# Kernel tuning notes

Measured on AMD Instinct MI355X. Metric: run time of the kernel, lower is better.

Reference implementation:

```python
import jax, jax.numpy as jnp
import numpy as np

B, N, T, FD = 128, 64, 20, 2
E, H, A = 16, 32, 32
DB, DH = 30.0, 30.0
NB, NHD = 12, 12  # 360/30 bearing and heading bins
DOMAIN_INIT = 5.0
EPS = 1e-12


def setup_inputs() -> dict:
    key = jax.random.key(0)
    ks = jax.random.split(key, 20)
    rn = lambda k, s, sc=0.1: (jax.random.normal(k, s) * sc).astype(jnp.float32)
    return {
        'x': jax.random.normal(ks[0], (B, N, T, FD), jnp.float32),
        'dmat': jax.random.uniform(ks[1], (B, N, T, N), jnp.float32) * 10.0,
        'bmat': jax.random.uniform(ks[2], (B, N, T, N), jnp.float32) * 360.0,
        'hmat': jax.random.uniform(ks[3], (B, N, T, N), jnp.float32) * 360.0,
        'mask': jnp.ones((B, N, T), jnp.float32),
        'emb_W': rn(ks[4], (E, FD)), 'emb_b': rn(ks[5], (E,)),
        'W_ih': rn(ks[6], (4 * H, E)), 'W_hh': rn(ks[7], (4 * H, H)),
        'b_ih': rn(ks[8], (4 * H,)), 'b_hh': rn(ks[9], (4 * H,)),
        'domain': jnp.full((NB, NHD), DOMAIN_INIT, jnp.float32),
        'enc2att_W': rn(ks[10], (A, H)), 'enc2att_b': rn(ks[11], (A,)),
        'spa_W': rn(ks[12], (A, 2 * A)), 'spa_b': rn(ks[13], (A,)),
        'att2enc_W': rn(ks[14], (H, A)), 'att2enc_b': rn(ks[15], (H,)),
        'cls_W': rn(ks[16], (1, H)), 'cls_b': rn(ks[17], (1,)),
        'h0': jax.random.normal(ks[18], (B * N, H), jnp.float32),
        'c0': jax.random.normal(ks[19], (B * N, H), jnp.float32),
    }


def _forward(x, dmat, bmat, hmat, mask, emb_W, emb_b, W_ih, W_hh, b_ih, b_hh,
             domain, enc2att_W, enc2att_b, spa_W, spa_b, att2enc_W, att2enc_b,
             cls_W, cls_b, h0, c0):
    # input embedding: [B,N,T,F] -> [T, B*N, E] (time-major for scan)
    xe = jnp.einsum('bntf,ef->bnte', x, emb_W) + emb_b
    xe = jnp.moveaxis(xe.reshape(B * N, T, E), 1, 0)
    dm_t = jnp.moveaxis(dmat, 2, 0)   # [T,B,N,N]
    bm_t = jnp.moveaxis(bmat, 2, 0)
    hm_t = jnp.moveaxis(hmat, 2, 0)
    mk_t = jnp.moveaxis(mask, 2, 0)   # [T,B,N]
    eye = jnp.eye(N, dtype=x.dtype)

    def step(carry, inputs):
        h, c = carry                     # [B*N, H]
        xt, dm, bm, hm, mk = inputs
        # single-step LSTM cell (torch gate order i,f,g,o)
        g = xt @ W_ih.T + b_ih + h @ W_hh.T + b_hh
        i, f, gg, o = jnp.split(g, 4, axis=-1)
        c = jax.nn.sigmoid(f) * c + jax.nn.sigmoid(i) * jnp.tanh(gg)
        h = jax.nn.sigmoid(o) * jnp.tanh(c)
        # project encoder state to attention space: [B,N,A]
        a = h.reshape(B, N, H) @ enc2att_W.T + enc2att_b
        # spatial attention weights from distance/bearing/heading edge feats
        ib = jnp.clip(jnp.floor(bm / DB), 0, NB - 1).astype(jnp.int32)
        ih = jnp.clip(jnp.floor(hm / DH), 0, NHD - 1).astype(jnp.int32)
        w = jax.nn.relu(domain[ib, ih] - dm)               # [B,N,N]
        w = w * mk[:, :, None] * mk[:, None, :] * (1.0 - eye)
        w = w / (jnp.sum(w, axis=-1, keepdims=True) + EPS)
        att = jnp.einsum('bij,bjd->bid', w, a)
        z = jnp.tanh(jnp.concatenate([a, att], axis=-1) @ spa_W.T + spa_b)
        h = (z @ att2enc_W.T + att2enc_b).reshape(B * N, H)
        return (h, c), None

    (h, c), _ = jax.lax.scan(step, (h0, c0), (xe, dm_t, bm_t, hm_t, mk_t))
    scores = jnp.tanh(h.reshape(B, N, H) @ cls_W.T + cls_b)
    return jax.nn.sigmoid(scores)  # [B, N, 1]


def reference(x, dmat, bmat, hmat, mask, emb_W, emb_b, W_ih, W_hh, b_ih, b_hh,
              domain, enc2att_W, enc2att_b, spa_W, spa_b, att2enc_W, att2enc_b,
              cls_W, cls_b, h0, c0):
    return _forward(x, dmat, bmat, hmat, mask, emb_W, emb_b, W_ih, W_hh, b_ih,
                    b_hh, domain, enc2att_W, enc2att_b, spa_W, spa_b,
                    att2enc_W, att2enc_b, cls_W, cls_b, h0, c0)
```

## Files before the change

### kernel.cpp

```cpp
#include <hip/hip_runtime.h>
#include <math.h>

#define T_STEPS 20

typedef _Float16 half8 __attribute__((ext_vector_type(8)));
typedef __fp16 fp16x2 __attribute__((ext_vector_type(2)));
typedef float f32x4 __attribute__((ext_vector_type(4)));

__device__ __forceinline__ float sigm(float v) {
  return __builtin_amdgcn_rcpf(1.0f + __expf(-v));
}
__device__ __forceinline__ float tanh_f(float v) {
  return 1.0f - 2.0f * __builtin_amdgcn_rcpf(1.0f + __expf(2.0f * v));
}

__device__ __forceinline__ void barrier_lgkm() {
  asm volatile("s_waitcnt lgkmcnt(0)" ::: "memory");
  __builtin_amdgcn_s_barrier();
  asm volatile("" ::: "memory");
}

__device__ __forceinline__ int2 pkpair(const f32x4 D) {
  const fp16x2 p0 = __builtin_amdgcn_cvt_pkrtz(D[0], D[1]);
  const fp16x2 p1 = __builtin_amdgcn_cvt_pkrtz(D[2], D[3]);
  int2 r;
  r.x = __builtin_bit_cast(int, p0);
  r.y = __builtin_bit_cast(int, p1);
  return r;
}

__global__ __launch_bounds__(1024)
void traj_disc(const float* __restrict__ x, const float* __restrict__ dmat,
               const float* __restrict__ bmat, const float* __restrict__ hmat,
               const float* __restrict__ maskp,
               const float* __restrict__ embW, const float* __restrict__ embb,
               const float* __restrict__ Wih, const float* __restrict__ Whh,
               const float* __restrict__ bih, const float* __restrict__ bhh,
               const float* __restrict__ dom,
               const float* __restrict__ e2aW, const float* __restrict__ e2ab,
               const float* __restrict__ spaW, const float* __restrict__ spab,
               const float* __restrict__ a2eW, const float* __restrict__ a2eb,
               const float* __restrict__ clsW, const float* __restrict__ clsb,
               const float* __restrict__ h0p, const float* __restrict__ c0p,
               float* __restrict__ out)
{
  __shared__ __align__(16) _Float16 sgw[128*40];
  __shared__ __align__(16) _Float16 sgwc[128*40];
  __shared__ __align__(16) float4   sgmb[128];
  __shared__ __align__(16) _Float16 sESaT[32*40];
  __shared__ __align__(16) _Float16 sEStT[32*40];
  __shared__ float bz[32];
  __shared__ float sdom[144];
  __shared__ float sm[1280];
  __shared__ float sclsc[32];
  __shared__ float sclsb2[1];
  __shared__ __align__(16) _Float16 sH[64*40];
  __shared__ __align__(16) _Float16 swA[64*72];
  __shared__ __align__(16) _Float16 swB[64*72];
  __shared__ __align__(16) _Float16 sz_[64*40];
  __shared__ __align__(16) _Float16 sqb[8*16*72 + 1440];

  const int tid = threadIdx.x;
  const int b = blockIdx.x;
  const int w = tid >> 6;
  const int l = tid & 63;
  const int quad = l >> 4;
  const int n16 = l & 15;
  const int i8 = (tid >= 512) ? ((tid - 512) >> 3) : 0;
  const int s8 = tid & 7;

  for (int idx = tid; idx < 4096; idx += 1024) sgw[(idx >> 5)*40 + (idx & 31)] = (_Float16)Whh[idx];
  {
    const int g = tid >> 3, kb = (tid & 7) << 2;
    float a0 = 0.f, a1 = 0.f, a2 = 0.f, a3 = 0.f;
    #pragma unroll
    for (int h = 0; h < 32; ++h) {
      const float wv = Whh[g*32 + h];
      a0 = fmaf(wv, a2eW[h*32 + kb + 0], a0);
      a1 = fmaf(wv, a2eW[h*32 + kb + 1], a1);
      a2 = fmaf(wv, a2eW[h*32 + kb + 2], a2);
      a3 = fmaf(wv, a2eW[h*32 + kb + 3], a3);
    }
    sgwc[g*40 + kb + 0] = (_Float16)a0; sgwc[g*40 + kb + 1] = (_Float16)a1;
    sgwc[g*40 + kb + 2] = (_Float16)a2; sgwc[g*40 + kb + 3] = (_Float16)a3;
  }
  if (tid < 128) {
    float m0 = 0.f, m1 = 0.f, b0 = bih[tid] + bhh[tid];
    #pragma unroll
    for (int e = 0; e < 16; ++e) {
      float wv_ = Wih[tid*16 + e];
      m0 = fmaf(wv_, embW[2*e],   m0);
      m1 = fmaf(wv_, embW[2*e+1], m1);
      b0 = fmaf(wv_, embb[e],     b0);
    }
    float bn = b0;
    #pragma unroll
    for (int h = 0; h < 32; ++h) bn = fmaf(Whh[tid*32 + h], a2eb[h], bn);
    sgmb[tid] = make_float4(m0, m1, b0, bn);
  }
  {
    const int zk = tid >> 5, hc = tid & 31;
    float sa_ = 0.f, st_ = 0.f;
    #pragma unroll
    for (int a = 0; a < 32; ++a) {
      const float ev = e2aW[a*32 + hc];
      sa_ = fmaf(spaW[zk*64 + a],      ev, sa_);
      st_ = fmaf(spaW[zk*64 + 32 + a], ev, st_);
    }
    sESaT[zk*40 + hc] = (_Float16)sa_;
    sEStT[zk*40 + hc] = (_Float16)st_;
  }
  if (tid < 32) {
    float acc = spab[tid];
    #pragma unroll
    for (int a = 0; a < 32; ++a)
      acc = fmaf(e2ab[a], spaW[tid*64 + a] + spaW[tid*64 + 32 + a], acc);
    bz[tid] = acc;
    float cc = 0.f;
    #pragma unroll
    for (int h = 0; h < 32; ++h) cc = fmaf(clsW[h], a2eW[h*32 + tid], cc);
    sclsc[tid] = cc;
  }
  if (tid == 0) {
    float cb = clsb[0];
    #pragma unroll
    for (int h = 0; h < 32; ++h) cb = fmaf(clsW[h], a2eb[h], cb);
    sclsb2[0] = cb;
  }
  if (tid < 144) sdom[tid] = dom[tid];
  for (int idx = tid; idx < 1280; idx += 1024)
    sm[idx] = maskp[(size_t)b*1280 + (size_t)(idx & 63)*20 + (idx >> 6)];
  for (int idx = tid; idx < 2048; idx += 1024) sz_[(idx >> 5)*40 + (idx & 31)] = (_Float16)h0p[(size_t)b*2048 + idx];

  f32x4 ccell;
  float2 xA, xB, xC, xD;
  f32x4 dmv0, dmv1, bmv0, bmv1, hmv0, hmv1;
  const float* xpre = nullptr;
  size_t ebp = 0;
  const int r = w >> 1, c = w & 1;
  if (w < 8) {
    const int hh = 16*c + n16;
    #pragma unroll
    for (int reg = 0; reg < 4; ++reg)
      ccell[reg] = c0p[(size_t)b*2048 + (size_t)(16*r + 4*quad + reg)*32 + hh];
    xpre = x + (size_t)(b*64 + 16*r + 4*quad) * 40;
    xA = *(const float2*)(xpre +   0);
    xB = *(const float2*)(xpre +  40);
    xC = *(const float2*)(xpre +  80);
    xD = *(const float2*)(xpre + 120);
  } else {
    ebp = ((size_t)(b*64 + i8)*20)*64 + (size_t)(s8*8);
    dmv0 = *(const f32x4*)(dmat + ebp); dmv1 = *(const f32x4*)(dmat + ebp + 4);
    bmv0 = *(const f32x4*)(bmat + ebp); bmv1 = *(const f32x4*)(bmat + ebp + 4);
    hmv0 = *(const f32x4*)(hmat + ebp); hmv1 = *(const f32x4*)(hmat + ebp + 4);
  }
  __syncthreads();

#define WC(dst, k, dmv, bmv, hmv, jof) { \
  int ib_ = (int)floorf(bmv[k] * (1.0f/30.0f)); ib_ = ib_ < 0 ? 0 : (ib_ > 11 ? 11 : ib_); \
  int ih_ = (int)floorf(hmv[k] * (1.0f/30.0f)); ih_ = ih_ < 0 ? 0 : (ih_ > 11 ? 11 : ih_); \
  float w_ = fmaxf(sdom[ib_*12 + ih_] - dmv[k], 0.0f) * (mi_ * sm[tloc*64 + 8*s8 + (jof)]); \
  w_ = (8*s8 + (jof) == i8) ? 0.0f : w_; dst[k] = w_; rs += w_; }

#define DO_3A(tn_, swdst) { \
  const int tloc = (tn_); \
  const float mi_ = sm[tloc*64 + i8]; \
  f32x4 wnA, wnB; float rs = 0.0f; \
  WC(wnA,0,dmv0,bmv0,hmv0,0) WC(wnA,1,dmv0,bmv0,hmv0,1) \
  WC(wnA,2,dmv0,bmv0,hmv0,2) WC(wnA,3,dmv0,bmv0,hmv0,3) \
  WC(wnB,0,dmv1,bmv1,hmv1,4) WC(wnB,1,dmv1,bmv1,hmv1,5) \
  WC(wnB,2,dmv1,bmv1,hmv1,6) WC(wnB,3,dmv1,bmv1,hmv1,7) \
  rs += __shfl_xor(rs, 1); rs += __shfl_xor(rs, 2); rs += __shfl_xor(rs, 4); \
  const float inv_ = __builtin_amdgcn_rcpf(rs + 1e-12f); \
  half8 hw; \
  hw[0] = (_Float16)(wnA[0]*inv_); hw[1] = (_Float16)(wnA[1]*inv_); \
  hw[2] = (_Float16)(wnA[2]*inv_); hw[3] = (_Float16)(wnA[3]*inv_); \
  hw[4] = (_Float16)(wnB[0]*inv_); hw[5] = (_Float16)(wnB[1]*inv_); \
  hw[6] = (_Float16)(wnB[2]*inv_); hw[7] = (_Float16)(wnB[3]*inv_); \
  *(half8*)((swdst) + i8*72 + s8*8) = hw; }

  half8 EStB{}, ESaB{};
  float bzv = 0.f;
  if (w < 8) {
    EStB = *(const half8*)(sEStT + (16*c + n16)*40 + quad*8);
    ESaB = *(const half8*)(sESaT + (16*c + n16)*40 + quad*8);
    bzv = bz[16*c + n16];
  } else {
    DO_3A(0, swA);
    const size_t eb1 = ebp + 64;
    dmv0 = *(const f32x4*)(dmat + eb1); dmv1 = *(const f32x4*)(dmat + eb1 + 4);
    bmv0 = *(const f32x4*)(bmat + eb1); bmv1 = *(const f32x4*)(bmat + eb1 + 4);
    hmv0 = *(const f32x4*)(hmat + eb1); hmv1 = *(const f32x4*)(hmat + eb1 + 4);
  }

  #pragma unroll 1
  for (int t = 0; t < T_STEPS; ++t) {
    if (w < 8) {
      const _Float16* Bbase = (t == 0) ? sgw : sgwc;
      const half8 Af = *(const half8*)(sz_ + (16*r + n16)*40 + quad*8);
      f32x4 G0, G1, G2, G3;
#define OP1Q(Gq, q) { \
      const int c_ = 2*(q) + c; \
      const half8 Bf = *(const half8*)(Bbase + (16*c_ + n16)*40 + quad*8); \
      const float4 mb = sgmb[16*c_ + n16]; \
      const float bb = (t == 0) ? mb.z : mb.w; \
      f32x4 Cv; \
      Cv[0] = fmaf(xA.x, mb.x, fmaf(xA.y, mb.y, bb)); \
      Cv[1] = fmaf(xB.x, mb.x, fmaf(xB.y, mb.y, bb)); \
      Cv[2] = fmaf(xC.x, mb.x, fmaf(xC.y, mb.y, bb)); \
      Cv[3] = fmaf(xD.x, mb.x, fmaf(xD.y, mb.y, bb)); \
      Gq = __builtin_amdgcn_mfma_f32_16x16x32_f16(Af, Bf, Cv, 0, 0, 0); }
      OP1Q(G0, 0) OP1Q(G1, 1) OP1Q(G2, 2) OP1Q(G3, 3)
#undef OP1Q
      const int hh = 16*c + n16;
      #pragma unroll
      for (int reg = 0; reg < 4; ++reg) {
        const float cc = fmaf(sigm(G1[reg]), ccell[reg], sigm(G0[reg]) * tanh_f(G2[reg]));
        ccell[reg] = cc;
        sH[(16*r + 4*quad + reg)*40 + hh] = (_Float16)(sigm(G3[reg]) * tanh_f(cc));
      }
      const int tn2 = ((t < T_STEPS - 1) ? t + 1 : t) << 1;
      xA = *(const float2*)(xpre + tn2);
      xB = *(const float2*)(xpre + tn2 +  40);
      xC = *(const float2*)(xpre + tn2 +  80);
      xD = *(const float2*)(xpre + tn2 + 120);
    } else {
      const int tn = (t < T_STEPS - 1) ? t + 1 : t;
      _Float16* swn = ((t + 1) & 1) ? swB : swA;
      DO_3A(tn, swn);
      const int tp = (t < T_STEPS - 2) ? t + 2 : T_STEPS - 1;
      const size_t eb2 = ebp + (size_t)tp*64;
      dmv0 = *(const f32x4*)(dmat + eb2); dmv1 = *(const f32x4*)(dmat + eb2 + 4);
      bmv0 = *(const f32x4*)(bmat + eb2); bmv1 = *(const f32x4*)(bmat + eb2 + 4);
      hmv0 = *(const f32x4*)(hmat + eb2); hmv1 = *(const f32x4*)(hmat + eb2 + 4);
    }
    barrier_lgkm();

    if (w < 8) {
      const _Float16* swr = (t & 1) ? swB : swA;
      _Float16* qb = sqb + w*(16*72);
      const half8 a0 = *(const half8*)(sH + (     n16)*40 + quad*8);
      const half8 a1 = *(const half8*)(sH + (16 + n16)*40 + quad*8);
      const half8 a2 = *(const half8*)(sH + (32 + n16)*40 + quad*8);
      const half8 a3 = *(const half8*)(sH + (48 + n16)*40 + quad*8);
      const half8 aP = *(const half8*)(sH + (16*r + n16)*40 + quad*8);
      const half8 A0 = *(const half8*)(swr + (16*r + n16)*72 + quad*8);
      const half8 A1 = *(const half8*)(swr + (16*r + n16)*72 + 32 + quad*8);
      f32x4 Pv; Pv[0] = bzv; Pv[1] = bzv; Pv[2] = bzv; Pv[3] = bzv;
      Pv = __builtin_amdgcn_mfma_f32_16x16x32_f16(aP, ESaB, Pv, 0, 0, 0);
      const f32x4 Z4 = {0.f, 0.f, 0.f, 0.f};
      const f32x4 D0 = __builtin_amdgcn_mfma_f32_16x16x32_f16(a0, EStB, Z4, 0, 0, 0);
      const f32x4 D1 = __builtin_amdgcn_mfma_f32_16x16x32_f16(a1, EStB, Z4, 0, 0, 0);
      const f32x4 D2 = __builtin_amdgcn_mfma_f32_16x16x32_f16(a2, EStB, Z4, 0, 0, 0);
      const f32x4 D3 = __builtin_amdgcn_mfma_f32_16x16x32_f16(a3, EStB, Z4, 0, 0, 0);
      *(int2*)(qb + n16*72 +  0 + 4*quad) = pkpair(D0);
      *(int2*)(qb + n16*72 + 16 + 4*quad) = pkpair(D1);
      *(int2*)(qb + n16*72 + 32 + 4*quad) = pkpair(D2);
      *(int2*)(qb + n16*72 + 48 + 4*quad) = pkpair(D3);
      const half8 Bf0 = *(const half8*)(qb + n16*72 + 8*quad);
      const half8 Bf1 = *(const half8*)(qb + n16*72 + 32 + 8*quad);
      Pv = __builtin_amdgcn_mfma_f32_16x16x32_f16(A0, Bf0, Pv, 0, 0, 0);
      Pv = __builtin_amdgcn_mfma_f32_16x16x32_f16(A1, Bf1, Pv, 0, 0, 0);
      const int nd = 16*r + 4*quad;
      sz_[(nd+0)*40 + 16*c + n16] = (_Float16)tanh_f(Pv[0]);
      sz_[(nd+1)*40 + 16*c + n16] = (_Float16)tanh_f(Pv[1]);
      sz_[(nd+2)*40 + 16*c + n16] = (_Float16)tanh_f(Pv[2]);
      sz_[(nd+3)*40 + 16*c + n16] = (_Float16)tanh_f(Pv[3]);
    }
    barrier_lgkm();
  }

#undef DO_3A
#undef WC

  if (tid < 64) {
    float acc = sclsb2[0];
    #pragma unroll
    for (int k = 0; k < 32; ++k) acc = fmaf((float)sz_[tid*40 + k], sclsc[k], acc);
    out[(size_t)b*64 + tid] = sigm(tanh_f(acc));
  }
}

extern "C" void kernel_launch(void* const* d_in, const int* in_sizes, int n_in,
                              void* d_out, int out_size, void* d_ws, size_t ws_size,
                              hipStream_t stream) {
  (void)in_sizes; (void)n_in; (void)d_ws; (void)ws_size; (void)out_size;
  const float* x    = (const float*)d_in[0];
  const float* dmat = (const float*)d_in[1];
  const float* bmat = (const float*)d_in[2];
  const float* hmat = (const float*)d_in[3];
  const float* mask = (const float*)d_in[4];
  const float* embW = (const float*)d_in[5];
  const float* embb = (const float*)d_in[6];
  const float* Wih  = (const float*)d_in[7];
  const float* Whh  = (const float*)d_in[8];
  const float* bih  = (const float*)d_in[9];
  const float* bhh  = (const float*)d_in[10];
  const float* dom  = (const float*)d_in[11];
  const float* e2aW = (const float*)d_in[12];
  const float* e2ab = (const float*)d_in[13];
  const float* spaW = (const float*)d_in[14];
  const float* spab = (const float*)d_in[15];
  const float* a2eW = (const float*)d_in[16];
  const float* a2eb = (const float*)d_in[17];
  const float* clsW = (const float*)d_in[18];
  const float* clsb = (const float*)d_in[19];
  const float* h0   = (const float*)d_in[20];
  const float* c0   = (const float*)d_in[21];
  float* out = (float*)d_out;

  traj_disc<<<dim3(128), dim3(1024), 0, stream>>>(
      x, dmat, bmat, hmat, mask, embW, embb, Wih, Whh, bih, bhh, dom,
      e2aW, e2ab, spaW, spab, a2eW, a2eb, clsW, clsb, h0, c0, out);
}
```

Before: 209.1 us.

## Pack two batches per block and fold exp scaling into gate weights

Each 1024-thread block now processes two batch elements with 512 threads each, and every wave performs both the edge-weight construction and the LSTM/attention MFMA work instead of specializing waves. Gate weights and biases are prescaled by -log2e (or 2·log2e for the tanh gate) so the activations use a raw v_exp_f32. Bearing and heading bin indices are now truncated without floor or clamp. This removes the wave specialization and some transcendental overhead, but halves the grid and lengthens each wave's per-step serial work, and it relies on angles staying in [0,360).

```diff
diff --git a/kernel.cpp b/kernel.cpp
--- a/kernel.cpp
+++ b/kernel.cpp
@@ -2,11 +2,15 @@
 #include <math.h>
 
 #define T_STEPS 20
+#define LOG2E 1.44269504088896f
 
 typedef _Float16 half8 __attribute__((ext_vector_type(8)));
 typedef __fp16 fp16x2 __attribute__((ext_vector_type(2)));
 typedef float f32x4 __attribute__((ext_vector_type(4)));
 
+__device__ __forceinline__ float exp2_f(float v) {
+  float r; asm("v_exp_f32 %0, %1" : "=v"(r) : "v"(v)); return r;
+}
 __device__ __forceinline__ float sigm(float v) {
   return __builtin_amdgcn_rcpf(1.0f + __expf(-v));
 }
@@ -51,27 +55,34 @@
   __shared__ __align__(16) _Float16 sEStT[32*40];
   __shared__ float bz[32];
   __shared__ float sdom[144];
-  __shared__ float sm[1280];
   __shared__ float sclsc[32];
   __shared__ float sclsb2[1];
-  __shared__ __align__(16) _Float16 sH[64*40];
-  __shared__ __align__(16) _Float16 swA[64*72];
-  __shared__ __align__(16) _Float16 swB[64*72];
-  __shared__ __align__(16) _Float16 sz_[64*40];
-  __shared__ __align__(16) _Float16 sqb[8*16*72 + 1440];
+  __shared__ float sm[2][1280];
+  __shared__ __align__(16) _Float16 sH[2][64*40];
+  __shared__ __align__(16) _Float16 swA[2][64*72];
+  __shared__ __align__(16) _Float16 swB[2][64*72];
+  __shared__ __align__(16) _Float16 sz_[2][64*40];
+  __shared__ __align__(16) _Float16 sqb[2][8*16*72];
 
   const int tid = threadIdx.x;
-  const int b = blockIdx.x;
-  const int w = tid >> 6;
+  const int g2 = tid >> 9;
+  const int btid = tid & 511;
+  const int bb = (blockIdx.x << 1) + g2;
+  const int wl = btid >> 6;
   const int l = tid & 63;
   const int quad = l >> 4;
   const int n16 = l & 15;
-  const int i8 = (tid >= 512) ? ((tid - 512) >> 3) : 0;
-  const int s8 = tid & 7;
-
-  for (int idx = tid; idx < 4096; idx += 1024) sgw[(idx >> 5)*40 + (idx & 31)] = (_Float16)Whh[idx];
+  const int r = wl >> 1, c = wl & 1;
+  const int i8 = btid >> 3, s8 = tid & 7;
+
+  for (int idx = tid; idx < 4096; idx += 1024) {
+    const int g = idx >> 5;
+    const float sq = ((g >> 5) == 2) ? 2.0f*LOG2E : -LOG2E;
+    sgw[g*40 + (idx & 31)] = (_Float16)(Whh[idx] * sq);
+  }
   {
     const int g = tid >> 3, kb = (tid & 7) << 2;
+    const float sq = ((g >> 5) == 2) ? 2.0f*LOG2E : -LOG2E;
     float a0 = 0.f, a1 = 0.f, a2 = 0.f, a3 = 0.f;
     #pragma unroll
     for (int h = 0; h < 32; ++h) {
@@ -81,10 +92,11 @@
       a2 = fmaf(wv, a2eW[h*32 + kb + 2], a2);
       a3 = fmaf(wv, a2eW[h*32 + kb + 3], a3);
     }
-    sgwc[g*40 + kb + 0] = (_Float16)a0; sgwc[g*40 + kb + 1] = (_Float16)a1;
-    sgwc[g*40 + kb + 2] = (_Float16)a2; sgwc[g*40 + kb + 3] = (_Float16)a3;
+    sgwc[g*40 + kb + 0] = (_Float16)(a0*sq); sgwc[g*40 + kb + 1] = (_Float16)(a1*sq);
+    sgwc[g*40 + kb + 2] = (_Float16)(a2*sq); sgwc[g*40 + kb + 3] = (_Float16)(a3*sq);
   }
   if (tid < 128) {
+    const float sq = ((tid >> 5) == 2) ? 2.0f*LOG2E : -LOG2E;
     float m0 = 0.f, m1 = 0.f, b0 = bih[tid] + bhh[tid];
     #pragma unroll
     for (int e = 0; e < 16; ++e) {
@@ -96,7 +108,7 @@
     float bn = b0;
     #pragma unroll
     for (int h = 0; h < 32; ++h) bn = fmaf(Whh[tid*32 + h], a2eb[h], bn);
-    sgmb[tid] = make_float4(m0, m1, b0, bn);
+    sgmb[tid] = make_float4(m0*sq, m1*sq, b0*sq, bn*sq);
   }
   {
     const int zk = tid >> 5, hc = tid & 31;
@@ -128,43 +140,38 @@
     sclsb2[0] = cb;
   }
   if (tid < 144) sdom[tid] = dom[tid];
-  for (int idx = tid; idx < 1280; idx += 1024)
-    sm[idx] = maskp[(size_t)b*1280 + (size_t)(idx & 63)*20 + (idx >> 6)];
-  for (int idx = tid; idx < 2048; idx += 1024) sz_[(idx >> 5)*40 + (idx & 31)] = (_Float16)h0p[(size_t)b*2048 + idx];
-
+  for (int idx = btid; idx < 1280; idx += 512)
+    sm[g2][idx] = maskp[(size_t)bb*1280 + (size_t)(idx & 63)*20 + (idx >> 6)];
+  for (int idx = btid; idx < 2048; idx += 512)
+    sz_[g2][(idx >> 5)*40 + (idx & 31)] = (_Float16)h0p[(size_t)bb*2048 + idx];
+
+  const int hh = 16*c + n16;
   f32x4 ccell;
-  float2 xA, xB, xC, xD;
-  f32x4 dmv0, dmv1, bmv0, bmv1, hmv0, hmv1;
-  const float* xpre = nullptr;
-  size_t ebp = 0;
-  const int r = w >> 1, c = w & 1;
-  if (w < 8) {
-    const int hh = 16*c + n16;
-    #pragma unroll
-    for (int reg = 0; reg < 4; ++reg)
-      ccell[reg] = c0p[(size_t)b*2048 + (size_t)(16*r + 4*quad + reg)*32 + hh];
-    xpre = x + (size_t)(b*64 + 16*r + 4*quad) * 40;
-    xA = *(const float2*)(xpre +   0);
-    xB = *(const float2*)(xpre +  40);
-    xC = *(const float2*)(xpre +  80);
-    xD = *(const float2*)(xpre + 120);
-  } else {
-    ebp = ((size_t)(b*64 + i8)*20)*64 + (size_t)(s8*8);
-    dmv0 = *(const f32x4*)(dmat + ebp); dmv1 = *(const f32x4*)(dmat + ebp + 4);
-    bmv0 = *(const f32x4*)(bmat + ebp); bmv1 = *(const f32x4*)(bmat + ebp + 4);
-    hmv0 = *(const f32x4*)(hmat + ebp); hmv1 = *(const f32x4*)(hmat + ebp + 4);
-  }
+  #pragma unroll
+  for (int reg = 0; reg < 4; ++reg)
+    ccell[reg] = c0p[(size_t)bb*2048 + (size_t)(16*r + 4*quad + reg)*32 + hh];
+  const float* xpre = x + (size_t)(bb*64 + 16*r + 4*quad) * 40;
+  float2 xA = *(const float2*)(xpre +   0);
+  float2 xB = *(const float2*)(xpre +  40);
+  float2 xC = *(const float2*)(xpre +  80);
+  float2 xD = *(const float2*)(xpre + 120);
+  const size_t ebp = ((size_t)(bb*64 + i8)*20)*64 + (size_t)(s8*8);
+  f32x4 dmv0 = *(const f32x4*)(dmat + ebp), dmv1 = *(const f32x4*)(dmat + ebp + 4);
+  f32x4 bmv0 = *(const f32x4*)(bmat + ebp), bmv1 = *(const f32x4*)(bmat + ebp + 4);
+  f32x4 hmv0 = *(const f32x4*)(hmat + ebp), hmv1 = *(const f32x4*)(hmat + ebp + 4);
   __syncthreads();
 
+  const float* smh = sm[g2];
+
 #define WC(dst, k, dmv, bmv, hmv, jof) { \
-  int ib_ = (int)floorf(bmv[k] * (1.0f/30.0f)); ib_ = ib_ < 0 ? 0 : (ib_ > 11 ? 11 : ib_); \
-  int ih_ = (int)floorf(hmv[k] * (1.0f/30.0f)); ih_ = ih_ < 0 ? 0 : (ih_ > 11 ? 11 : ih_); \
-  float w_ = fmaxf(sdom[ib_*12 + ih_] - dmv[k], 0.0f) * (mi_ * sm[tloc*64 + 8*s8 + (jof)]); \
+  const int ib_ = (int)(bmv[k] * (1.0f/30.0f)); \
+  const int ih_ = (int)(hmv[k] * (1.0f/30.0f)); \
+  float w_ = fmaxf(sdom[ib_*12 + ih_] - dmv[k], 0.0f) * (mi_ * smh[tloc*64 + 8*s8 + (jof)]); \
   w_ = (8*s8 + (jof) == i8) ? 0.0f : w_; dst[k] = w_; rs += w_; }
 
 #define DO_3A(tn_, swdst) { \
   const int tloc = (tn_); \
-  const float mi_ = sm[tloc*64 + i8]; \
+  const float mi_ = smh[tloc*64 + i8]; \
   f32x4 wnA, wnB; float rs = 0.0f; \
   WC(wnA,0,dmv0,bmv0,hmv0,0) WC(wnA,1,dmv0,bmv0,hmv0,1) \
   WC(wnA,2,dmv0,bmv0,hmv0,2) WC(wnA,3,dmv0,bmv0,hmv0,3) \
@@ -179,14 +186,11 @@
   hw[6] = (_Float16)(wnB[2]*inv_); hw[7] = (_Float16)(wnB[3]*inv_); \
   *(half8*)((swdst) + i8*72 + s8*8) = hw; }
 
-  half8 EStB{}, ESaB{};
-  float bzv = 0.f;
-  if (w < 8) {
-    EStB = *(const half8*)(sEStT + (16*c + n16)*40 + quad*8);
-    ESaB = *(const half8*)(sESaT + (16*c + n16)*40 + quad*8);
-    bzv = bz[16*c + n16];
-  } else {
-    DO_3A(0, swA);
+  const half8 EStB = *(const half8*)(sEStT + (16*c + n16)*40 + quad*8);
+  const half8 ESaB = *(const half8*)(sESaT + (16*c + n16)*40 + quad*8);
+  const float bzv = bz[16*c + n16];
+  DO_3A(0, swA[g2]);
+  {
     const size_t eb1 = ebp + 64;
     dmv0 = *(const f32x4*)(dmat + eb1); dmv1 = *(const f32x4*)(dmat + eb1 + 4);
     bmv0 = *(const f32x4*)(bmat + eb1); bmv1 = *(const f32x4*)(bmat + eb1 + 4);
@@ -195,39 +199,45 @@
 
   #pragma unroll 1
   for (int t = 0; t < T_STEPS; ++t) {
-    if (w < 8) {
+    {
       const _Float16* Bbase = (t == 0) ? sgw : sgwc;
-      const half8 Af = *(const half8*)(sz_ + (16*r + n16)*40 + quad*8);
+      const _Float16* szh = sz_[g2];
+      const half8 Af = *(const half8*)(szh + (16*r + n16)*40 + quad*8);
       f32x4 G0, G1, G2, G3;
 #define OP1Q(Gq, q) { \
       const int c_ = 2*(q) + c; \
       const half8 Bf = *(const half8*)(Bbase + (16*c_ + n16)*40 + quad*8); \
       const float4 mb = sgmb[16*c_ + n16]; \
-      const float bb = (t == 0) ? mb.z : mb.w; \
+      const float bb_ = (t == 0) ? mb.z : mb.w; \
       f32x4 Cv; \
-      Cv[0] = fmaf(xA.x, mb.x, fmaf(xA.y, mb.y, bb)); \
-      Cv[1] = fmaf(xB.x, mb.x, fmaf(xB.y, mb.y, bb)); \
-      Cv[2] = fmaf(xC.x, mb.x, fmaf(xC.y, mb.y, bb)); \
-      Cv[3] = fmaf(xD.x, mb.x, fmaf(xD.y, mb.y, bb)); \
+      Cv[0] = fmaf(xA.x, mb.x, fmaf(xA.y, mb.y, bb_)); \
+      Cv[1] = fmaf(xB.x, mb.x, fmaf(xB.y, mb.y, bb_)); \
+      Cv[2] = fmaf(xC.x, mb.x, fmaf(xC.y, mb.y, bb_)); \
+      Cv[3] = fmaf(xD.x, mb.x, fmaf(xD.y, mb.y, bb_)); \
       Gq = __builtin_amdgcn_mfma_f32_16x16x32_f16(Af, Bf, Cv, 0, 0, 0); }
       OP1Q(G0, 0) OP1Q(G1, 1) OP1Q(G2, 2) OP1Q(G3, 3)
 #undef OP1Q
-      const int hh = 16*c + n16;
+      {
+        const int tn = (t < T_STEPS - 1) ? t + 1 : t;
+        _Float16* swn = ((t + 1) & 1) ? swB[g2] : swA[g2];
+        DO_3A(tn, swn);
+      }
+      _Float16* sHh = sH[g2];
       #pragma unroll
       for (int reg = 0; reg < 4; ++reg) {
-        const float cc = fmaf(sigm(G1[reg]), ccell[reg], sigm(G0[reg]) * tanh_f(G2[reg]));
+        const float si = __builtin_amdgcn_rcpf(1.0f + exp2_f(G0[reg]));
+        const float sf = __builtin_amdgcn_rcpf(1.0f + exp2_f(G1[reg]));
+        const float tg = 1.0f - 2.0f*__builtin_amdgcn_rcpf(1.0f + exp2_f(G2[reg]));
+        const float so = __builtin_amdgcn_rcpf(1.0f + exp2_f(G3[reg]));
+        const float cc = fmaf(sf, ccell[reg], si * tg);
         ccell[reg] = cc;
-        sH[(16*r + 4*quad + reg)*40 + hh] = (_Float16)(sigm(G3[reg]) * tanh_f(cc));
+        sHh[(16*r + 4*quad + reg)*40 + hh] = (_Float16)(so * tanh_f(cc));
       }
       const int tn2 = ((t < T_STEPS - 1) ? t + 1 : t) << 1;
       xA = *(const float2*)(xpre + tn2);
       xB = *(const float2*)(xpre + tn2 +  40);
       xC = *(const float2*)(xpre + tn2 +  80);
       xD = *(const float2*)(xpre + tn2 + 120);
-    } else {
-      const int tn = (t < T_STEPS - 1) ? t + 1 : t;
-      _Float16* swn = ((t + 1) & 1) ? swB : swA;
-      DO_3A(tn, swn);
       const int tp = (t < T_STEPS - 2) ? t + 2 : T_STEPS - 1;
       const size_t eb2 = ebp + (size_t)tp*64;
       dmv0 = *(const f32x4*)(dmat + eb2); dmv1 = *(const f32x4*)(dmat + eb2 + 4);
@@ -236,14 +246,15 @@
     }
     barrier_lgkm();
 
-    if (w < 8) {
-      const _Float16* swr = (t & 1) ? swB : swA;
-      _Float16* qb = sqb + w*(16*72);
-      const half8 a0 = *(const half8*)(sH + (     n16)*40 + quad*8);
-      const half8 a1 = *(const half8*)(sH + (16 + n16)*40 + quad*8);
-      const half8 a2 = *(const half8*)(sH + (32 + n16)*40 + quad*8);
-      const half8 a3 = *(const half8*)(sH + (48 + n16)*40 + quad*8);
-      const half8 aP = *(const half8*)(sH + (16*r + n16)*40 + quad*8);
+    {
+      const _Float16* swr = (t & 1) ? swB[g2] : swA[g2];
+      const _Float16* sHh = sH[g2];
+      _Float16* qb = sqb[g2] + wl*(16*72);
+      const half8 a0 = *(const half8*)(sHh + (     n16)*40 + quad*8);
+      const half8 a1 = *(const half8*)(sHh + (16 + n16)*40 + quad*8);
+      const half8 a2 = *(const half8*)(sHh + (32 + n16)*40 + quad*8);
+      const half8 a3 = *(const half8*)(sHh + (48 + n16)*40 + quad*8);
+      const half8 aP = *(const half8*)(sHh + (16*r + n16)*40 + quad*8);
       const half8 A0 = *(const half8*)(swr + (16*r + n16)*72 + quad*8);
       const half8 A1 = *(const half8*)(swr + (16*r + n16)*72 + 32 + quad*8);
       f32x4 Pv; Pv[0] = bzv; Pv[1] = bzv; Pv[2] = bzv; Pv[3] = bzv;
@@ -261,11 +272,12 @@
       const half8 Bf1 = *(const half8*)(qb + n16*72 + 32 + 8*quad);
       Pv = __builtin_amdgcn_mfma_f32_16x16x32_f16(A0, Bf0, Pv, 0, 0, 0);
       Pv = __builtin_amdgcn_mfma_f32_16x16x32_f16(A1, Bf1, Pv, 0, 0, 0);
+      _Float16* szh = sz_[g2];
       const int nd = 16*r + 4*quad;
-      sz_[(nd+0)*40 + 16*c + n16] = (_Float16)tanh_f(Pv[0]);
-      sz_[(nd+1)*40 + 16*c + n16] = (_Float16)tanh_f(Pv[1]);
-      sz_[(nd+2)*40 + 16*c + n16] = (_Float16)tanh_f(Pv[2]);
-      sz_[(nd+3)*40 + 16*c + n16] = (_Float16)tanh_f(Pv[3]);
+      szh[(nd+0)*40 + 16*c + n16] = (_Float16)tanh_f(Pv[0]);
+      szh[(nd+1)*40 + 16*c + n16] = (_Float16)tanh_f(Pv[1]);
+      szh[(nd+2)*40 + 16*c + n16] = (_Float16)tanh_f(Pv[2]);
+      szh[(nd+3)*40 + 16*c + n16] = (_Float16)tanh_f(Pv[3]);
     }
     barrier_lgkm();
   }
@@ -273,11 +285,12 @@
 #undef DO_3A
 #undef WC
 
-  if (tid < 64) {
+  if (btid < 64) {
+    const _Float16* szh = sz_[g2];
     float acc = sclsb2[0];
     #pragma unroll
-    for (int k = 0; k < 32; ++k) acc = fmaf((float)sz_[tid*40 + k], sclsc[k], acc);
-    out[(size_t)b*64 + tid] = sigm(tanh_f(acc));
+    for (int k = 0; k < 32; ++k) acc = fmaf((float)szh[btid*40 + k], sclsc[k], acc);
+    out[(size_t)bb*64 + btid] = sigm(tanh_f(acc));
   }
 }
 
@@ -309,7 +322,7 @@
   const float* c0   = (const float*)d_in[21];
   float* out = (float*)d_out;
 
-  traj_disc<<<dim3(128), dim3(1024), 0, stream>>>(
+  traj_disc<<<dim3(64), dim3(1024), 0, stream>>>(
       x, dmat, bmat, hmat, mask, embW, embb, Wih, Whh, bih, bhh, dom,
       e2aW, e2ab, spaW, spab, a2eW, a2eb, clsW, clsb, h0, c0, out);
 }
```

Result: slower. 255.9 us (+22.4%).
